# Kernel optimization log

Hardware: AMD Instinct MI355X
Metric: run time of the kernel (lower is better)

The kernel has to match this reference:

```python
import jax, jax.numpy as jnp
import numpy as np

N_NODES = 100000
N_EDGES = 1600000
D_IN, D_HID, D_OUT = 128, 128, 40


def _degrees(src, dst, n):
    ones = jnp.ones((src.shape[0],), dtype=jnp.float32)
    out_deg = jax.ops.segment_sum(ones, src, num_segments=n)
    in_deg = jax.ops.segment_sum(ones, dst, num_segments=n)
    # DGL clamps zero degrees to 1 to avoid inf
    return jnp.maximum(out_deg, 1.0), jnp.maximum(in_deg, 1.0)


def _graph_conv(x, W, b, src, dst, out_norm, in_norm, n):
    # norm='both': h = D_in^{-1/2} * A^T * (D_out^{-1/2} * x W) + b
    h = x @ W                      # [N, d_out] (W applied first: d_in >= d_out)
    h = h * out_norm[:, None]      # scale source features
    agg = jax.ops.segment_sum(h[src], dst, num_segments=n)  # gather-scatter SpMM
    return agg * in_norm[:, None] + b


def setup_inputs() -> dict:
    key = jax.random.key(0)
    ks = jax.random.split(key, 8)
    x = jax.random.normal(ks[0], (N_NODES, D_IN), dtype=jnp.float32)
    edge_index = jax.random.randint(ks[1], (2, N_EDGES), 0, N_NODES, dtype=jnp.int32)
    def glorot(k, fan_in, fan_out):
        lim = np.sqrt(6.0 / (fan_in + fan_out)).astype(np.float32)
        return jax.random.uniform(k, (fan_in, fan_out), jnp.float32, -lim, lim)
    return {
        "x": x,
        "edge_index": edge_index,
        "W1": glorot(ks[2], D_IN, D_HID), "b1": jnp.zeros((D_HID,), jnp.float32),
        "W2": glorot(ks[3], D_HID, D_HID), "b2": jnp.zeros((D_HID,), jnp.float32),
        "W3": glorot(ks[4], D_HID, D_OUT), "b3": jnp.zeros((D_OUT,), jnp.float32),
    }


def reference(x, edge_index, W1, b1, W2, b2, W3, b3):
    src, dst = edge_index[0], edge_index[1]
    out_deg, in_deg = _degrees(src, dst, N_NODES)
    out_norm = jax.lax.rsqrt(out_deg)
    in_norm = jax.lax.rsqrt(in_deg)
    h = _graph_conv(x, W1, b1, src, dst, out_norm, in_norm, N_NODES)
    h = jax.nn.relu(h)  # dropout inactive at inference
    h = _graph_conv(h, W2, b2, src, dst, out_norm, in_norm, N_NODES)
    h = jax.nn.relu(h)
    h = _graph_conv(h, W3, b3, src, dst, out_norm, in_norm, N_NODES)
    return jax.nn.log_softmax(h, axis=-1)
```

## Files before the change

### kernel.cpp

```cpp
#include <hip/hip_runtime.h>
#include <hip/hip_bf16.h>
#include <math.h>

typedef __hip_bfloat16 bf16;
typedef __attribute__((ext_vector_type(8))) short short8v;
typedef __attribute__((ext_vector_type(4))) float f32x4;

#define ELLW 64
#define NPB 256
#define NBMAX 512
#define CAPB 8192
#define CHUNKA 8192

__device__ __forceinline__ float bflo(unsigned u) { return __uint_as_float(u << 16); }
__device__ __forceinline__ float bfhi(unsigned u) { return __uint_as_float(u & 0xffff0000u); }
__device__ __forceinline__ unsigned short f2bf(float f) {
    unsigned u = __float_as_uint(f);
    return (unsigned short)((u + 0x7fff + ((u >> 16) & 1)) >> 16);
}


__device__ __forceinline__ void pack_one(const float* __restrict__ W, bf16* __restrict__ Wb,
                                         int idx, int NOUT, int NPAD) {
    int r = idx & 7;
    int rest = idx >> 3;
    int col = rest % NPAD;
    int sk = rest / NPAD;
    int k = sk * 8 + r;
    float v = (col < NOUT) ? W[k * NOUT + col] : 0.0f;
    Wb[idx] = __float2bfloat16(v);
}

__global__ void pack_all(const float* __restrict__ W1, const float* __restrict__ W2,
                         const float* __restrict__ W3, bf16* __restrict__ Wb1,
                         bf16* __restrict__ Wb2, bf16* __restrict__ Wb3) {
    int idx = blockIdx.x * blockDim.x + threadIdx.x;
    if (idx < 16384) pack_one(W1, Wb1, idx, 128, 128);
    else if (idx < 32768) pack_one(W2, Wb2, idx - 16384, 128, 128);
    else if (idx < 40960) pack_one(W3, Wb3, idx - 32768, 40, 64);
}


template <int NT>
__device__ void gemm_body_f32(int bid, const float* __restrict__ Af,
                              const bf16* __restrict__ Wb, bf16* __restrict__ H, int n) {
    constexpr int NPAD = NT * 16;
    int lane = threadIdx.x & 63;
    int wid = threadIdx.x >> 6;
    int base = (bid * 4 + wid) * 16;
    if (base >= n) return;
    int m = lane & 15, kb = lane >> 4;
    int arow = base + m;

    short8v az = {0, 0, 0, 0, 0, 0, 0, 0};
    short8v a[4];
    const float4* apf = (const float4*)(Af + (size_t)arow * 128);
#pragma unroll
    for (int s = 0; s < 4; ++s) {
        short8v w = az;
        if (arow < n) {
            float4 p = apf[s * 8 + kb * 2];
            float4 q = apf[s * 8 + kb * 2 + 1];
            w[0] = (short)f2bf(p.x); w[1] = (short)f2bf(p.y);
            w[2] = (short)f2bf(p.z); w[3] = (short)f2bf(p.w);
            w[4] = (short)f2bf(q.x); w[5] = (short)f2bf(q.y);
            w[6] = (short)f2bf(q.z); w[7] = (short)f2bf(q.w);
        }
        a[s] = w;
    }

    f32x4 zz = {0.f, 0.f, 0.f, 0.f};
    f32x4 acc[NT];
#pragma unroll
    for (int t = 0; t < NT; ++t) acc[t] = zz;

    const short8v* bp = (const short8v*)Wb;
#pragma unroll
    for (int s = 0; s < 4; ++s) {
#pragma unroll
        for (int t = 0; t < NT; ++t) {
            short8v b = bp[(size_t)(s * 4 + kb) * NPAD + t * 16 + m];
            acc[t] = __builtin_amdgcn_mfma_f32_16x16x32_bf16(a[s], b, acc[t], 0, 0, 0);
        }
    }

    int orow0 = base + kb * 4;
#pragma unroll
    for (int r = 0; r < 4; ++r) {
        int rr = orow0 + r;
        if (rr < n) {
#pragma unroll
            for (int t = 0; t < NT; ++t)
                H[(size_t)rr * NPAD + t * 16 + m] = __float2bfloat16(acc[t][r]);
        }
    }
}


__device__ void scatter_body(int bid, const int* __restrict__ src, const int* __restrict__ dst,
                             int nbk, int* __restrict__ gCurD, int* __restrict__ gCurS,
                             unsigned* __restrict__ pairD, int* __restrict__ srcS, int E) {
    __shared__ int histD[NBMAX], histS[NBMAX], offD[NBMAX], offS[NBMAX];
    int tid = threadIdx.x;
    int base = bid * CHUNKA;
    int cnt = E - base; if (cnt > CHUNKA) cnt = CHUNKA;
    for (int i = tid; i < nbk; i += 256) { histD[i] = 0; histS[i] = 0; }
    __syncthreads();
#pragma unroll
    for (int j = 0; j < CHUNKA / 1024; ++j) {
        int i0 = (j * 256 + tid) * 4;
        if (i0 + 3 < cnt) {
            int4 s4 = *(const int4*)(src + base + i0);
            int4 d4 = *(const int4*)(dst + base + i0);
            atomicAdd(&histD[d4.x >> 8], 1); atomicAdd(&histS[s4.x >> 8], 1);
            atomicAdd(&histD[d4.y >> 8], 1); atomicAdd(&histS[s4.y >> 8], 1);
            atomicAdd(&histD[d4.z >> 8], 1); atomicAdd(&histS[s4.z >> 8], 1);
            atomicAdd(&histD[d4.w >> 8], 1); atomicAdd(&histS[s4.w >> 8], 1);
        } else {
            for (int i = i0; i < cnt && i < i0 + 4; ++i) {
                atomicAdd(&histD[dst[base + i] >> 8], 1);
                atomicAdd(&histS[src[base + i] >> 8], 1);
            }
        }
    }
    __syncthreads();
    for (int i = tid; i < nbk; i += 256) {
        offD[i] = atomicAdd(&gCurD[i], histD[i]);
        offS[i] = atomicAdd(&gCurS[i], histS[i]);
    }
    __syncthreads();
    for (int i = tid; i < nbk; i += 256) { histD[i] = 0; histS[i] = 0; }
    __syncthreads();
#pragma unroll
    for (int j = 0; j < CHUNKA / 1024; ++j) {
        int i0 = (j * 256 + tid) * 4;
        int lim = cnt - i0; if (lim > 4) lim = 4;
        if (lim > 0) {
            int ss[4], dd[4];
            if (lim == 4) {
                int4 s4 = *(const int4*)(src + base + i0);
                int4 d4 = *(const int4*)(dst + base + i0);
                ss[0] = s4.x; ss[1] = s4.y; ss[2] = s4.z; ss[3] = s4.w;
                dd[0] = d4.x; dd[1] = d4.y; dd[2] = d4.z; dd[3] = d4.w;
            } else {
                for (int i = 0; i < lim; ++i) { ss[i] = src[base + i0 + i]; dd[i] = dst[base + i0 + i]; }
            }
            for (int i = 0; i < lim; ++i) {
                int bd = dd[i] >> 8;
                int p = atomicAdd(&histD[bd], 1) + offD[bd];
                if (p < CAPB)
                    pairD[(size_t)bd * CAPB + p] = ((unsigned)(dd[i] & 255) << 17) | (unsigned)ss[i];
                int bs = ss[i] >> 8;
                int q = atomicAdd(&histS[bs], 1) + offS[bs];
                if (q < CAPB) srcS[(size_t)bs * CAPB + q] = ss[i];
            }
        }
    }
}


__global__ void phase1(const int* __restrict__ src, const int* __restrict__ dst,
                       int nbk, int* __restrict__ gCurD, int* __restrict__ gCurS,
                       unsigned* __restrict__ pairD, int* __restrict__ srcS, int E,
                       int scatterBlocks, const float* __restrict__ x,
                       const bf16* __restrict__ Wb1, bf16* __restrict__ H, int n) {
    if ((int)blockIdx.x < scatterBlocks)
        scatter_body(blockIdx.x, src, dst, nbk, gCurD, gCurS, pairD, srcS, E);
    else
        gemm_body_f32<8>(blockIdx.x - scatterBlocks, x, Wb1, H, n);
}


__global__ void phase2(const unsigned* __restrict__ pairD, const int* __restrict__ srcS,
                       const int* __restrict__ gCurD, const int* __restrict__ gCurS,
                       int* __restrict__ ell, int* __restrict__ cnt_in,
                       float* __restrict__ innf, float* __restrict__ outn, int nbk, int n) {
    int bid = blockIdx.x;
    int tid = threadIdx.x;
    if (bid < nbk) {
        __shared__ int cnt[NPB];
        cnt[tid & (NPB - 1)] = 0;
        __syncthreads();
        int m = gCurD[bid]; if (m > CAPB) m = CAPB;
        const unsigned* p = pairD + (size_t)bid * CAPB;
        int nb0 = bid << 8;
        for (int i = tid; i < m; i += 256) {
            unsigned v = p[i];
            int local = (int)(v >> 17);
            int s = (int)(v & 0x1FFFF);
            int pos = atomicAdd(&cnt[local], 1);
            if (pos < ELLW) ell[((size_t)(nb0 + local) << 6) + pos] = s;
        }
        __syncthreads();
        int node = nb0 + tid;
        if (tid < NPB && node < n) {
            cnt_in[node] = cnt[tid];
            innf[node] = rsqrtf(fmaxf((float)cnt[tid], 1.0f));
        }
    } else {
        int b = bid - nbk;
        __shared__ int cnt2[NPB];
        cnt2[tid & (NPB - 1)] = 0;
        __syncthreads();
        int m = gCurS[b]; if (m > CAPB) m = CAPB;
        const int* p = srcS + (size_t)b * CAPB;
        int nb0 = b << 8;
        for (int i = tid; i < m; i += 256)
            atomicAdd(&cnt2[p[i] - nb0], 1);
        __syncthreads();
        int node = nb0 + tid;
        if (tid < NPB && node < n)
            outn[node] = rsqrtf(fmaxf((float)cnt2[tid], 1.0f));
    }
}


template <int NT, bool EDGE_OUTN>
__global__ void gather_gemm_fused(const bf16* __restrict__ h, const int* __restrict__ cnt_in,
                                  const int* __restrict__ ell, const float* __restrict__ outn,
                                  const float* __restrict__ inn, const float* __restrict__ bias,
                                  const bf16* __restrict__ Wb, bf16* __restrict__ H, int n) {
    constexpr int NPAD = NT * 16;
    constexpr int NTW = NT / 4;
    __shared__ short rows[16][136];
    int lane = threadIdx.x & 63;
    int wid = threadIdx.x >> 6;
    int nodeBase = blockIdx.x * 16;
    const unsigned* hu = (const unsigned*)h;

#pragma unroll
    for (int q = 0; q < 4; ++q) {
        int r = wid * 4 + q;
        int node = nodeBase + r;
        unsigned pk = 0;
        if (node < n) {
            int d = min(cnt_in[node], ELLW);
            const int4* row4 = (const int4*)(ell + ((size_t)node << 6));
            const int* row = (const int*)row4;
            float a0 = 0.f, a1 = 0.f, a2 = 0.f, a3 = 0.f;
            float a4 = 0.f, a5 = 0.f, a6 = 0.f, a7 = 0.f;
            int k = 0;
            for (; k + 7 < d; k += 8) {
                int kq = k >> 2;
                int4 q0 = row4[kq], q1 = row4[kq + 1];
                unsigned u0 = hu[((size_t)q0.x << 6) + lane];
                unsigned u1 = hu[((size_t)q0.y << 6) + lane];
                unsigned u2 = hu[((size_t)q0.z << 6) + lane];
                unsigned u3 = hu[((size_t)q0.w << 6) + lane];
                unsigned u4 = hu[((size_t)q1.x << 6) + lane];
                unsigned u5 = hu[((size_t)q1.y << 6) + lane];
                unsigned u6 = hu[((size_t)q1.z << 6) + lane];
                unsigned u7 = hu[((size_t)q1.w << 6) + lane];
                if constexpr (EDGE_OUTN) {
                    float o0 = outn[q0.x], o1 = outn[q0.y], o2 = outn[q0.z], o3 = outn[q0.w];
                    float o4 = outn[q1.x], o5 = outn[q1.y], o6 = outn[q1.z], o7 = outn[q1.w];
                    a0 += o0 * bflo(u0); a1 += o0 * bfhi(u0);
                    a2 += o1 * bflo(u1); a3 += o1 * bfhi(u1);
                    a4 += o2 * bflo(u2); a5 += o2 * bfhi(u2);
                    a6 += o3 * bflo(u3); a7 += o3 * bfhi(u3);
                    a0 += o4 * bflo(u4); a1 += o4 * bfhi(u4);
                    a2 += o5 * bflo(u5); a3 += o5 * bfhi(u5);
                    a4 += o6 * bflo(u6); a5 += o6 * bfhi(u6);
                    a6 += o7 * bflo(u7); a7 += o7 * bfhi(u7);
                } else {
                    a0 += bflo(u0); a1 += bfhi(u0);
                    a2 += bflo(u1); a3 += bfhi(u1);
                    a4 += bflo(u2); a5 += bfhi(u2);
                    a6 += bflo(u3); a7 += bfhi(u3);
                    a0 += bflo(u4); a1 += bfhi(u4);
                    a2 += bflo(u5); a3 += bfhi(u5);
                    a4 += bflo(u6); a5 += bfhi(u6);
                    a6 += bflo(u7); a7 += bfhi(u7);
                }
            }
            for (; k + 3 < d; k += 4) {
                int4 q0 = row4[k >> 2];
                unsigned u0 = hu[((size_t)q0.x << 6) + lane];
                unsigned u1 = hu[((size_t)q0.y << 6) + lane];
                unsigned u2 = hu[((size_t)q0.z << 6) + lane];
                unsigned u3 = hu[((size_t)q0.w << 6) + lane];
                if constexpr (EDGE_OUTN) {
                    float o0 = outn[q0.x], o1 = outn[q0.y], o2 = outn[q0.z], o3 = outn[q0.w];
                    a0 += o0 * bflo(u0); a1 += o0 * bfhi(u0);
                    a2 += o1 * bflo(u1); a3 += o1 * bfhi(u1);
                    a4 += o2 * bflo(u2); a5 += o2 * bfhi(u2);
                    a6 += o3 * bflo(u3); a7 += o3 * bfhi(u3);
                } else {
                    a0 += bflo(u0); a1 += bfhi(u0);
                    a2 += bflo(u1); a3 += bfhi(u1);
                    a4 += bflo(u2); a5 += bfhi(u2);
                    a6 += bflo(u3); a7 += bfhi(u3);
                }
            }
            for (; k < d; ++k) {
                int e = row[k];
                unsigned u = hu[((size_t)e << 6) + lane];
                if constexpr (EDGE_OUTN) {
                    float o = outn[e];
                    a0 += o * bflo(u); a1 += o * bfhi(u);
                } else {
                    a0 += bflo(u); a1 += bfhi(u);
                }
            }
            float innv = inn[node];
            float2 bb = ((const float2*)bias)[lane];
            float f0 = fmaxf(((a0 + a2) + (a4 + a6)) * innv + bb.x, 0.0f);
            float f1 = fmaxf(((a1 + a3) + (a5 + a7)) * innv + bb.y, 0.0f);
            pk = (unsigned)f2bf(f0) | ((unsigned)f2bf(f1) << 16);
        }
        ((unsigned*)rows[r])[lane] = pk;
    }
    __syncthreads();

    if (NT == 4 && wid == 3) return;
    int m = lane & 15, kb = lane >> 4;
    short8v a[4];
#pragma unroll
    for (int s = 0; s < 4; ++s)
        a[s] = *(const short8v*)&rows[m][s * 32 + kb * 8];

    f32x4 zz = {0.f, 0.f, 0.f, 0.f};
    f32x4 acc[NTW];
#pragma unroll
    for (int t = 0; t < NTW; ++t) acc[t] = zz;

    const short8v* bp = (const short8v*)Wb;
#pragma unroll
    for (int s = 0; s < 4; ++s) {
#pragma unroll
        for (int t = 0; t < NTW; ++t) {
            int tt = wid * NTW + t;
            short8v b = bp[(size_t)(s * 4 + kb) * NPAD + tt * 16 + m];
            acc[t] = __builtin_amdgcn_mfma_f32_16x16x32_bf16(a[s], b, acc[t], 0, 0, 0);
        }
    }

    int orow0 = nodeBase + kb * 4;
#pragma unroll
    for (int r = 0; r < 4; ++r) {
        int rr = orow0 + r;
        if (rr < n) {
            float sc = outn[rr];
#pragma unroll
            for (int t = 0; t < NTW; ++t)
                H[(size_t)rr * NPAD + (wid * NTW + t) * 16 + m] = __float2bfloat16(acc[t][r] * sc);
        }
    }
}


__global__ void gather40_lsm_p64(const bf16* __restrict__ h, const int* __restrict__ cnt_in,
                                 const int* __restrict__ ell,
                                 const float* __restrict__ inn, const float* __restrict__ b,
                                 float* __restrict__ out, int n) {
    int node = blockIdx.x * 4 + (threadIdx.x >> 6);
    int lane = threadIdx.x & 63;
    if (node >= n) return;
    int d = min(cnt_in[node], ELLW);
    const int* row = ell + ((size_t)node << 6);
    int grp = lane >> 5;
    int l = lane & 31;
    const unsigned* hu = (const unsigned*)h;
    float a0 = 0.f, a1 = 0.f, a2 = 0.f, a3 = 0.f;
    int k = grp;
    for (; k + 14 < d; k += 16) {
        int e0 = row[k],      e1 = row[k + 2],  e2 = row[k + 4],  e3 = row[k + 6];
        int e4 = row[k + 8],  e5 = row[k + 10], e6 = row[k + 12], e7 = row[k + 14];
        unsigned u0 = hu[((size_t)e0 << 5) + l];
        unsigned u1 = hu[((size_t)e1 << 5) + l];
        unsigned u2 = hu[((size_t)e2 << 5) + l];
        unsigned u3 = hu[((size_t)e3 << 5) + l];
        unsigned u4 = hu[((size_t)e4 << 5) + l];
        unsigned u5 = hu[((size_t)e5 << 5) + l];
        unsigned u6 = hu[((size_t)e6 << 5) + l];
        unsigned u7 = hu[((size_t)e7 << 5) + l];
        a0 += bflo(u0); a1 += bfhi(u0);
        a2 += bflo(u1); a3 += bfhi(u1);
        a0 += bflo(u2); a1 += bfhi(u2);
        a2 += bflo(u3); a3 += bfhi(u3);
        a0 += bflo(u4); a1 += bfhi(u4);
        a2 += bflo(u5); a3 += bfhi(u5);
        a0 += bflo(u6); a1 += bfhi(u6);
        a2 += bflo(u7); a3 += bfhi(u7);
    }
    for (; k + 6 < d; k += 8) {
        int e0 = row[k], e1 = row[k + 2], e2 = row[k + 4], e3 = row[k + 6];
        unsigned u0 = hu[((size_t)e0 << 5) + l];
        unsigned u1 = hu[((size_t)e1 << 5) + l];
        unsigned u2 = hu[((size_t)e2 << 5) + l];
        unsigned u3 = hu[((size_t)e3 << 5) + l];
        a0 += bflo(u0); a1 += bfhi(u0);
        a2 += bflo(u1); a3 += bfhi(u1);
        a0 += bflo(u2); a1 += bfhi(u2);
        a2 += bflo(u3); a3 += bfhi(u3);
    }
    for (; k + 2 < d; k += 4) {
        int e0 = row[k], e1 = row[k + 2];
        unsigned u0 = hu[((size_t)e0 << 5) + l];
        unsigned u1 = hu[((size_t)e1 << 5) + l];
        a0 += bflo(u0); a1 += bfhi(u0);
        a2 += bflo(u1); a3 += bfhi(u1);
    }
    if (k < d) {
        int e = row[k];
        unsigned u = hu[((size_t)e << 5) + l];
        a0 += bflo(u); a1 += bfhi(u);
    }
    a0 += a2; a1 += a3;
    a0 += __shfl_xor(a0, 32);
    a1 += __shfl_xor(a1, 32);
    float innv = inn[node];
    bool act = (l < 20);
    float2 bb = act ? ((const float2*)b)[l] : make_float2(0.f, 0.f);
    float v0 = act ? (a0 * innv + bb.x) : -INFINITY;
    float v1 = act ? (a1 * innv + bb.y) : -INFINITY;
    float m = fmaxf(v0, v1);
#pragma unroll
    for (int o = 16; o; o >>= 1) m = fmaxf(m, __shfl_xor(m, o));
    float e = act ? (expf(v0 - m) + expf(v1 - m)) : 0.0f;
#pragma unroll
    for (int o = 16; o; o >>= 1) e += __shfl_xor(e, o);
    float ls = m + logf(e);
    if (act && grp == 0)
        ((float2*)(out + (size_t)node * 40))[l] = make_float2(v0 - ls, v1 - ls);
}


extern "C" void kernel_launch(void* const* d_in, const int* in_sizes, int n_in,
                              void* d_out, int out_size, void* d_ws, size_t ws_size,
                              hipStream_t stream) {
    const float* x  = (const float*)d_in[0];
    const int*   ei = (const int*)d_in[1];
    const float* W1 = (const float*)d_in[2];
    const float* b1 = (const float*)d_in[3];
    const float* W2 = (const float*)d_in[4];
    const float* b2 = (const float*)d_in[5];
    const float* W3 = (const float*)d_in[6];
    const float* b3 = (const float*)d_in[7];

    const int n = in_sizes[0] / 128;
    const int E = in_sizes[1] / 2;
    const int* src = ei;
    const int* dst = ei + E;
    const int nbk = (n + NPB - 1) / NPB;

    char* wsb = (char*)d_ws;
    size_t off = 0;
    auto alloc = [&](size_t bytes) { void* p = wsb + off; off = (off + bytes + 63) & ~(size_t)63; return p; };
    float*    outn    = (float*)alloc((size_t)n * 4);
    float*    innf    = (float*)alloc((size_t)n * 4);
    int*      cnt_in  = (int*)alloc((size_t)n * 4);
    int*      gCurD   = (int*)alloc((size_t)nbk * 4);
    int*      gCurS   = (int*)alloc((size_t)nbk * 4);
    int*      ell     = (int*)alloc((size_t)n * ELLW * 4);
    unsigned* pairD   = (unsigned*)alloc((size_t)nbk * CAPB * 4);
    bf16*     Wb1     = (bf16*)alloc(16 * 128 * 8 * 2);
    bf16*     Wb2     = (bf16*)alloc(16 * 128 * 8 * 2);
    bf16*     Wb3     = (bf16*)alloc(16 * 64 * 8 * 2);
    bf16*     hb      = (bf16*)alloc((size_t)n * 128 * 2);
    bf16*     gb      = (bf16*)alloc((size_t)n * 128 * 2);
    int*      srcS    = (int*)gb;

    hipMemsetAsync(gCurD, 0, ((size_t)((char*)gCurS - (char*)gCurD) + (size_t)nbk * 4), stream);

    pack_all<<<(40960 + 255) / 256, 256, 0, stream>>>(W1, W2, W3, Wb1, Wb2, Wb3);

    const int scatterBlocks = (E + CHUNKA - 1) / CHUNKA;
    const int gemmBlocks = (n + 63) / 64;
    phase1<<<scatterBlocks + gemmBlocks, 256, 0, stream>>>(src, dst, nbk, gCurD, gCurS, pairD,
                                                           srcS, E, scatterBlocks, x, Wb1, hb, n);
    phase2<<<2 * nbk, 256, 0, stream>>>(pairD, srcS, gCurD, gCurS, ell, cnt_in, innf, outn,
                                        nbk, n);

    const int fblk = (n + 15) / 16;
    gather_gemm_fused<8, true><<<fblk, 256, 0, stream>>>(hb, cnt_in, ell, outn, innf, b1,
                                                         Wb2, gb, n);
    gather_gemm_fused<4, false><<<fblk, 256, 0, stream>>>(gb, cnt_in, ell, outn, innf, b2,
                                                          Wb3, hb, n);
    gather40_lsm_p64<<<(n + 3) / 4, 256, 0, stream>>>(hb, cnt_in, ell, innf, b3,
                                                      (float*)d_out, n);
}
```

Before: 263.5 us.

## Unfuse gather and GEMM, gather from feature-sliced layout for L2 locality

After: 566.0 us. 115% more time.

```diff
diff --git a/kernel.cpp b/kernel.cpp
--- a/kernel.cpp
+++ b/kernel.cpp
@@ -91,7 +91,57 @@
         if (rr < n) {
 #pragma unroll
             for (int t = 0; t < NT; ++t)
-                H[(size_t)rr * NPAD + t * 16 + m] = __float2bfloat16(acc[t][r]);
+                H[((size_t)t * n + rr) * 16 + m] = __float2bfloat16(acc[t][r]);
+        }
+    }
+}
+
+
+template <int NT, int NTUSE, bool SLICEOUT>
+__global__ void gemm_bf16k(const bf16* __restrict__ A, const bf16* __restrict__ Wb,
+                           const float* __restrict__ outn, bf16* __restrict__ H, int n) {
+    constexpr int NPAD = NT * 16;
+    int lane = threadIdx.x & 63;
+    int wid = threadIdx.x >> 6;
+    int base = (blockIdx.x * 4 + wid) * 16;
+    if (base >= n) return;
+    int m = lane & 15, kb = lane >> 4;
+    int arow = base + m;
+
+    short8v az = {0, 0, 0, 0, 0, 0, 0, 0};
+    short8v a[4];
+    const short8v* ap = (const short8v*)(A + (size_t)arow * 128);
+#pragma unroll
+    for (int s = 0; s < 4; ++s)
+        a[s] = (arow < n) ? ap[s * 4 + kb] : az;
+
+    f32x4 zz = {0.f, 0.f, 0.f, 0.f};
+    f32x4 acc[NTUSE];
+#pragma unroll
+    for (int t = 0; t < NTUSE; ++t) acc[t] = zz;
+
+    const short8v* bp = (const short8v*)Wb;
+#pragma unroll
+    for (int s = 0; s < 4; ++s) {
+#pragma unroll
+        for (int t = 0; t < NTUSE; ++t) {
+            short8v b = bp[(size_t)(s * 4 + kb) * NPAD + t * 16 + m];
+            acc[t] = __builtin_amdgcn_mfma_f32_16x16x32_bf16(a[s], b, acc[t], 0, 0, 0);
+        }
+    }
+
+    int orow0 = base + kb * 4;
+#pragma unroll
+    for (int r = 0; r < 4; ++r) {
+        int rr = orow0 + r;
+        if (rr < n) {
+            float sc = outn[rr];
+#pragma unroll
+            for (int t = 0; t < NTUSE; ++t) {
+                bf16 v = __float2bfloat16(acc[t][r] * sc);
+                if constexpr (SLICEOUT) H[((size_t)t * n + rr) * 16 + m] = v;
+                else                    H[(size_t)rr * NPAD + t * 16 + m] = v;
+            }
         }
     }
 }
@@ -215,135 +265,59 @@
 }
 
 
-template <int NT, bool EDGE_OUTN>
-__global__ void gather_gemm_fused(const bf16* __restrict__ h, const int* __restrict__ cnt_in,
-                                  const int* __restrict__ ell, const float* __restrict__ outn,
-                                  const float* __restrict__ inn, const float* __restrict__ bias,
-                                  const bf16* __restrict__ Wb, bf16* __restrict__ H, int n) {
-    constexpr int NPAD = NT * 16;
-    constexpr int NTW = NT / 4;
-    __shared__ short rows[16][136];
+template <bool EDGE_OUTN>
+__global__ void sgather128(const bf16* __restrict__ hS, const int* __restrict__ cnt_in,
+                           const int* __restrict__ ell, const float* __restrict__ outn,
+                           const float* __restrict__ inn, const float* __restrict__ bias,
+                           unsigned* __restrict__ out, int n) {
+    int slice = blockIdx.x & 7;
+    int chunk = blockIdx.x >> 3;
     int lane = threadIdx.x & 63;
     int wid = threadIdx.x >> 6;
-    int nodeBase = blockIdx.x * 16;
-    const unsigned* hu = (const unsigned*)h;
-
+    int sg = lane >> 3, li = lane & 7;
+    const unsigned* hu = (const unsigned*)hS + (size_t)slice * n * 8;
 #pragma unroll
     for (int q = 0; q < 4; ++q) {
-        int r = wid * 4 + q;
-        int node = nodeBase + r;
-        unsigned pk = 0;
-        if (node < n) {
-            int d = min(cnt_in[node], ELLW);
-            const int4* row4 = (const int4*)(ell + ((size_t)node << 6));
-            const int* row = (const int*)row4;
-            float a0 = 0.f, a1 = 0.f, a2 = 0.f, a3 = 0.f;
-            float a4 = 0.f, a5 = 0.f, a6 = 0.f, a7 = 0.f;
-            int k = 0;
-            for (; k + 7 < d; k += 8) {
-                int kq = k >> 2;
-                int4 q0 = row4[kq], q1 = row4[kq + 1];
-                unsigned u0 = hu[((size_t)q0.x << 6) + lane];
-                unsigned u1 = hu[((size_t)q0.y << 6) + lane];
-                unsigned u2 = hu[((size_t)q0.z << 6) + lane];
-                unsigned u3 = hu[((size_t)q0.w << 6) + lane];
-                unsigned u4 = hu[((size_t)q1.x << 6) + lane];
-                unsigned u5 = hu[((size_t)q1.y << 6) + lane];
-                unsigned u6 = hu[((size_t)q1.z << 6) + lane];
-                unsigned u7 = hu[((size_t)q1.w << 6) + lane];
-                if constexpr (EDGE_OUTN) {
-                    float o0 = outn[q0.x], o1 = outn[q0.y], o2 = outn[q0.z], o3 = outn[q0.w];
-                    float o4 = outn[q1.x], o5 = outn[q1.y], o6 = outn[q1.z], o7 = outn[q1.w];
-                    a0 += o0 * bflo(u0); a1 += o0 * bfhi(u0);
-                    a2 += o1 * bflo(u1); a3 += o1 * bfhi(u1);
-                    a4 += o2 * bflo(u2); a5 += o2 * bfhi(u2);
-                    a6 += o3 * bflo(u3); a7 += o3 * bfhi(u3);
-                    a0 += o4 * bflo(u4); a1 += o4 * bfhi(u4);
-                    a2 += o5 * bflo(u5); a3 += o5 * bfhi(u5);
-                    a4 += o6 * bflo(u6); a5 += o6 * bfhi(u6);
-                    a6 += o7 * bflo(u7); a7 += o7 * bfhi(u7);
-                } else {
-                    a0 += bflo(u0); a1 += bfhi(u0);
-                    a2 += bflo(u1); a3 += bfhi(u1);
-                    a4 += bflo(u2); a5 += bfhi(u2);
-                    a6 += bflo(u3); a7 += bfhi(u3);
-                    a0 += bflo(u4); a1 += bfhi(u4);
-                    a2 += bflo(u5); a3 += bfhi(u5);
-                    a4 += bflo(u6); a5 += bfhi(u6);
-                    a6 += bflo(u7); a7 += bfhi(u7);
-                }
-            }
-            for (; k + 3 < d; k += 4) {
-                int4 q0 = row4[k >> 2];
-                unsigned u0 = hu[((size_t)q0.x << 6) + lane];
-                unsigned u1 = hu[((size_t)q0.y << 6) + lane];
-                unsigned u2 = hu[((size_t)q0.z << 6) + lane];
-                unsigned u3 = hu[((size_t)q0.w << 6) + lane];
-                if constexpr (EDGE_OUTN) {
-                    float o0 = outn[q0.x], o1 = outn[q0.y], o2 = outn[q0.z], o3 = outn[q0.w];
-                    a0 += o0 * bflo(u0); a1 += o0 * bfhi(u0);
-                    a2 += o1 * bflo(u1); a3 += o1 * bfhi(u1);
-                    a4 += o2 * bflo(u2); a5 += o2 * bfhi(u2);
-                    a6 += o3 * bflo(u3); a7 += o3 * bfhi(u3);
-                } else {
-                    a0 += bflo(u0); a1 += bfhi(u0);
-                    a2 += bflo(u1); a3 += bfhi(u1);
-                    a4 += bflo(u2); a5 += bfhi(u2);
-                    a6 += bflo(u3); a7 += bfhi(u3);
-                }
-            }
-            for (; k < d; ++k) {
-                int e = row[k];
-                unsigned u = hu[((size_t)e << 6) + lane];
-                if constexpr (EDGE_OUTN) {
-                    float o = outn[e];
-                    a0 += o * bflo(u); a1 += o * bfhi(u);
-                } else {
-                    a0 += bflo(u); a1 += bfhi(u);
-                }
-            }
+        int node = chunk * 16 + wid * 4 + q;
+        if (node >= n) break;
+        int d = min(cnt_in[node], ELLW);
+        const int* row = ell + ((size_t)node << 6);
+        float a0 = 0.f, a1 = 0.f, c0 = 0.f, c1 = 0.f;
+        int k = sg;
+        for (; k + 8 < d; k += 16) {
+            int e0 = row[k], e1 = row[k + 8];
+            unsigned u0 = hu[((size_t)e0 << 3) + li];
+            unsigned u1 = hu[((size_t)e1 << 3) + li];
+            if constexpr (EDGE_OUTN) {
+                float o0 = outn[e0], o1 = outn[e1];
+                a0 += o0 * bflo(u0); a1 += o0 * bfhi(u0);
+                c0 += o1 * bflo(u1); c1 += o1 * bfhi(u1);
+            } else {
+                a0 += bflo(u0); a1 += bfhi(u0);
+                c0 += bflo(u1); c1 += bfhi(u1);
+            }
+        }
+        if (k < d) {
+            int e = row[k];
+            unsigned u = hu[((size_t)e << 3) + li];
+            if constexpr (EDGE_OUTN) {
+                float o = outn[e];
+                a0 += o * bflo(u); a1 += o * bfhi(u);
+            } else {
+                a0 += bflo(u); a1 += bfhi(u);
+            }
+        }
+        a0 += c0; a1 += c1;
+        a0 += __shfl_xor(a0, 8);  a1 += __shfl_xor(a1, 8);
+        a0 += __shfl_xor(a0, 16); a1 += __shfl_xor(a1, 16);
+        a0 += __shfl_xor(a0, 32); a1 += __shfl_xor(a1, 32);
+        if (sg == 0) {
             float innv = inn[node];
-            float2 bb = ((const float2*)bias)[lane];
-            float f0 = fmaxf(((a0 + a2) + (a4 + a6)) * innv + bb.x, 0.0f);
-            float f1 = fmaxf(((a1 + a3) + (a5 + a7)) * innv + bb.y, 0.0f);
-            pk = (unsigned)f2bf(f0) | ((unsigned)f2bf(f1) << 16);
-        }
-        ((unsigned*)rows[r])[lane] = pk;
-    }
-    __syncthreads();
-
-    if (NT == 4 && wid == 3) return;
-    int m = lane & 15, kb = lane >> 4;
-    short8v a[4];
-#pragma unroll
-    for (int s = 0; s < 4; ++s)
-        a[s] = *(const short8v*)&rows[m][s * 32 + kb * 8];
-
-    f32x4 zz = {0.f, 0.f, 0.f, 0.f};
-    f32x4 acc[NTW];
-#pragma unroll
-    for (int t = 0; t < NTW; ++t) acc[t] = zz;
-
-    const short8v* bp = (const short8v*)Wb;
-#pragma unroll
-    for (int s = 0; s < 4; ++s) {
-#pragma unroll
-        for (int t = 0; t < NTW; ++t) {
-            int tt = wid * NTW + t;
-            short8v b = bp[(size_t)(s * 4 + kb) * NPAD + tt * 16 + m];
-            acc[t] = __builtin_amdgcn_mfma_f32_16x16x32_bf16(a[s], b, acc[t], 0, 0, 0);
-        }
-    }
-
-    int orow0 = nodeBase + kb * 4;
-#pragma unroll
-    for (int r = 0; r < 4; ++r) {
-        int rr = orow0 + r;
-        if (rr < n) {
-            float sc = outn[rr];
-#pragma unroll
-            for (int t = 0; t < NTW; ++t)
-                H[(size_t)rr * NPAD + (wid * NTW + t) * 16 + m] = __float2bfloat16(acc[t][r] * sc);
+            float2 bb = ((const float2*)bias)[slice * 8 + li];
+            float f0 = fmaxf(a0 * innv + bb.x, 0.0f);
+            float f1 = fmaxf(a1 * innv + bb.y, 0.0f);
+            out[(size_t)node * 64 + slice * 8 + li] =
+                (unsigned)f2bf(f0) | ((unsigned)f2bf(f1) << 16);
         }
     }
 }
@@ -457,9 +431,9 @@
     bf16*     Wb1     = (bf16*)alloc(16 * 128 * 8 * 2);
     bf16*     Wb2     = (bf16*)alloc(16 * 128 * 8 * 2);
     bf16*     Wb3     = (bf16*)alloc(16 * 64 * 8 * 2);
-    bf16*     hb      = (bf16*)alloc((size_t)n * 128 * 2);
-    bf16*     gb      = (bf16*)alloc((size_t)n * 128 * 2);
-    int*      srcS    = (int*)gb;
+    bf16*     hbS     = (bf16*)alloc((size_t)n * 128 * 2);
+    bf16*     B       = (bf16*)alloc((size_t)n * 128 * 2);
+    int*      srcS    = (int*)B;
 
     hipMemsetAsync(gCurD, 0, ((size_t)((char*)gCurS - (char*)gCurD) + (size_t)nbk * 4), stream);
 
@@ -468,15 +442,17 @@
     const int scatterBlocks = (E + CHUNKA - 1) / CHUNKA;
     const int gemmBlocks = (n + 63) / 64;
     phase1<<<scatterBlocks + gemmBlocks, 256, 0, stream>>>(src, dst, nbk, gCurD, gCurS, pairD,
-                                                           srcS, E, scatterBlocks, x, Wb1, hb, n);
+                                                           srcS, E, scatterBlocks, x, Wb1, hbS, n);
     phase2<<<2 * nbk, 256, 0, stream>>>(pairD, srcS, gCurD, gCurS, ell, cnt_in, innf, outn,
                                         nbk, n);
 
-    const int fblk = (n + 15) / 16;
-    gather_gemm_fused<8, true><<<fblk, 256, 0, stream>>>(hb, cnt_in, ell, outn, innf, b1,
-                                                         Wb2, gb, n);
-    gather_gemm_fused<4, false><<<fblk, 256, 0, stream>>>(gb, cnt_in, ell, outn, innf, b2,
-                                                          Wb3, hb, n);
-    gather40_lsm_p64<<<(n + 3) / 4, 256, 0, stream>>>(hb, cnt_in, ell, innf, b3,
+    const int sblk = 8 * ((n + 15) / 16);
+    sgather128<true><<<sblk, 256, 0, stream>>>(hbS, cnt_in, ell, outn, innf, b1,
+                                               (unsigned*)B, n);
+    gemm_bf16k<8, 8, true><<<gemmBlocks, 256, 0, stream>>>(B, Wb2, outn, hbS, n);
+    sgather128<false><<<sblk, 256, 0, stream>>>(hbS, cnt_in, ell, outn, innf, b2,
+                                                (unsigned*)B, n);
+    gemm_bf16k<4, 3, false><<<gemmBlocks, 256, 0, stream>>>(B, Wb3, outn, hbS, n);
+    gather40_lsm_p64<<<(n + 3) / 4, 256, 0, stream>>>(hbS, cnt_in, ell, innf, b3,
                                                       (float*)d_out, n);
 }
```
